# Optimization experiments

Hardware: AMD Instinct MI355X
Metric: run time of the kernel (lower is better)

The kernel has to match this reference:

```python
import jax, jax.numpy as jnp
import numpy as np

BASE_LR = 0.1
LN_EPS = 1e-5
D_IN = 1024
D_OUT = 1024
BATCH = 16384


def setup_inputs() -> dict:
    key = jax.random.key(0)
    ks = jax.random.split(key, 5)
    x = jax.random.normal(ks[0], (BATCH, D_IN), dtype=jnp.float32)
    plasticity = jax.random.uniform(ks[1], (BATCH,), dtype=jnp.float32)
    alpha = jax.random.uniform(ks[2], (1,), dtype=jnp.float32)
    # Parameters / buffers (orthogonal / kaiming init approximated with scaled normals)
    W_slow = jax.random.normal(ks[3], (D_OUT, D_IN), dtype=jnp.float32) * (1.4 / np.sqrt(D_IN))
    bound = 1.0 / np.sqrt(D_IN)  # kaiming_uniform with a=sqrt(5) on [d_out, d_in]
    W_fast = jax.random.uniform(ks[4], (D_OUT, D_IN), dtype=jnp.float32, minval=-bound, maxval=bound)
    gamma = jnp.ones((D_OUT,), dtype=jnp.float32)
    beta = jnp.zeros((D_OUT,), dtype=jnp.float32)
    return {"x": x, "plasticity": plasticity, "alpha": alpha,
            "W_slow": W_slow, "W_fast": W_fast, "gamma": gamma, "beta": beta}


def reference(x, plasticity, alpha, W_slow, W_fast, gamma, beta):
    # Dual linear reads: [B, d_in] @ [d_in, d_out]
    slow = x @ W_slow.T           # [B, d_out]
    fast = x @ W_fast.T           # [B, d_out]

    # Hebbian fast-weight update (training branch, no-grad in original)
    batch = x.shape[0]
    hebb = (fast.T @ x) / batch                         # [d_out, d_in]
    forget = jnp.mean(fast ** 2, axis=0)[:, None] * W_fast  # [d_out, d_in]
    eff_lr = jnp.mean(plasticity) * BASE_LR             # scalar, kept on-device
    W_fast_new = W_fast + jnp.tanh(hebb - forget) * eff_lr

    # Combine + LayerNorm over last dim
    combined = slow + fast * alpha                      # alpha broadcast scalar
    mu = jnp.mean(combined, axis=-1, keepdims=True)
    var = jnp.mean((combined - mu) ** 2, axis=-1, keepdims=True)
    out = (combined - mu) * jax.lax.rsqrt(var + LN_EPS) * gamma + beta
    return (out, slow, W_fast_new)
```

## Files before the change

kernel.cpp:

```cpp
#include <hip/hip_runtime.h>
#include <cstdint>
#include <cstddef>

#define B_SZ 16384
#define DIN  1024
#define DOUT 1024
#define SPLITK 8

typedef short bf16x8 __attribute__((ext_vector_type(8)));
typedef float f32x4  __attribute__((ext_vector_type(4)));

static __device__ __forceinline__ short f2bf(float f) {
    union { float f; unsigned u; } v; v.f = f;
    unsigned r = v.u + 0x7fffu + ((v.u >> 16) & 1u);
    return (short)(r >> 16);
}
static __device__ __forceinline__ float bf2f(short s) {
    union { unsigned u; float f; } v; v.u = ((unsigned)(unsigned short)s) << 16;
    return v.f;
}
static __device__ __forceinline__ void gload_lds16(const short* g, short* l) {
    __builtin_amdgcn_global_load_lds(
        (const __attribute__((address_space(1))) void*)g,
        (__attribute__((address_space(3))) void*)l, 16, 0, 0);
}

__global__ __launch_bounds__(256) void convert_f32_bf16(const float* __restrict__ in,
                                                        short* __restrict__ out, int n4) {
    int i = blockIdx.x * 256 + threadIdx.x;
    if (i < n4) {
        float4 v = ((const float4*)in)[i];
        short4 o;
        o.x = f2bf(v.x); o.y = f2bf(v.y); o.z = f2bf(v.z); o.w = f2bf(v.w);
        ((short4*)out)[i] = o;
    }
}

__global__ __launch_bounds__(256) void x_convert(const float* __restrict__ x,
                                                 short* __restrict__ xb,
                                                 short* __restrict__ xT) {
    __shared__ short t[64 * 72];
    const int b0 = blockIdx.x * 64;
    const int d0 = blockIdx.y * 64;
    const int tid = threadIdx.x;
    const int r = tid >> 2;
    const int c = (tid & 3) * 16;
    short loc[16];
    #pragma unroll
    for (int i = 0; i < 4; ++i) {
        float4 v = *(const float4*)&x[(size_t)(b0 + r) * DIN + d0 + c + i * 4];
        loc[i * 4 + 0] = f2bf(v.x); loc[i * 4 + 1] = f2bf(v.y);
        loc[i * 4 + 2] = f2bf(v.z); loc[i * 4 + 3] = f2bf(v.w);
    }
    *(bf16x8*)&xb[(size_t)(b0 + r) * DIN + d0 + c]     = *(bf16x8*)&loc[0];
    *(bf16x8*)&xb[(size_t)(b0 + r) * DIN + d0 + c + 8] = *(bf16x8*)&loc[8];
    #pragma unroll
    for (int i = 0; i < 16; ++i) t[(c + i) * 72 + r] = loc[i];
    __syncthreads();
    const int d = tid >> 2, bs = (tid & 3) * 16;
    *(bf16x8*)&xT[(size_t)(d0 + d) * B_SZ + b0 + bs]     = *(bf16x8*)&t[d * 72 + bs];
    *(bf16x8*)&xT[(size_t)(d0 + d) * B_SZ + b0 + bs + 8] = *(bf16x8*)&t[d * 72 + bs + 8];
}

__global__ __launch_bounds__(256) void fast_trans(const float* __restrict__ fast,
                                                  short* __restrict__ fastT) {
    __shared__ short t[64 * 72];
    const int b0 = blockIdx.x * 64;
    const int d0 = blockIdx.y * 64;
    const int tid = threadIdx.x;
    const int r = tid >> 2;
    const int c = (tid & 3) * 16;
    short loc[16];
    #pragma unroll
    for (int i = 0; i < 4; ++i) {
        float4 v = *(const float4*)&fast[(size_t)(b0 + r) * DOUT + d0 + c + i * 4];
        loc[i * 4 + 0] = f2bf(v.x); loc[i * 4 + 1] = f2bf(v.y);
        loc[i * 4 + 2] = f2bf(v.z); loc[i * 4 + 3] = f2bf(v.w);
    }
    #pragma unroll
    for (int i = 0; i < 16; ++i) t[(c + i) * 72 + r] = loc[i];
    __syncthreads();
    const int d = tid >> 2, bs = (tid & 3) * 16;
    *(bf16x8*)&fastT[(size_t)(d0 + d) * B_SZ + b0 + bs]     = *(bf16x8*)&t[d * 72 + bs];
    *(bf16x8*)&fastT[(size_t)(d0 + d) * B_SZ + b0 + bs + 8] = *(bf16x8*)&t[d * 72 + bs + 8];
}

__global__ __launch_bounds__(256) void init_kernel(const float* __restrict__ plast,
                                                   float* __restrict__ eff_lr) {
    int tid = threadIdx.x;
    float s = 0.f;
    for (int i = tid; i < B_SZ; i += 256) s += plast[i];
    __shared__ float red[256];
    red[tid] = s; __syncthreads();
    for (int off = 128; off > 0; off >>= 1) {
        if (tid < off) red[tid] += red[tid + off];
        __syncthreads();
    }
    if (tid == 0) eff_lr[0] = (red[0] / (float)B_SZ) * 0.1f;
}

__global__ __launch_bounds__(256) void dual_gemm(
    const short* __restrict__ Xb,
    const short* __restrict__ Wc,
    float* __restrict__ slow_out,
    float* __restrict__ fast_out)
{
    __shared__ short lA[128 * 32];
    __shared__ short lB[128 * 32];
    const int tid = threadIdx.x;
    const int lane = tid & 63;
    const int wave = tid >> 6;
    const int wm = wave & 1, wn = wave >> 1;
    const int quad = lane >> 4, l16 = lane & 15;
    const int m0 = blockIdx.x * 128;
    const int n0 = blockIdx.y * 128;
    const int lrow = lane >> 2;
    const int lcol = (lane & 3) * 8;

    f32x4 acc[4][4] = {};

    const short* gA0 = &Xb[(size_t)(m0 + wave * 32 + lrow) * DIN + lcol];
    const short* gA1 = gA0 + (size_t)16 * DIN;
    const short* gB0 = &Wc[(size_t)(n0 + wave * 32 + lrow) * DIN + lcol];
    const short* gB1 = gB0 + (size_t)16 * DIN;
    short* sA0 = &lA[(wave * 32) * 32];
    short* sA1 = &lA[(wave * 32 + 16) * 32];
    short* sB0 = &lB[(wave * 32) * 32];
    short* sB1 = &lB[(wave * 32 + 16) * 32];

    for (int k0 = 0; k0 < DIN; k0 += 32) {
        gload_lds16(gA0 + k0, sA0);
        gload_lds16(gA1 + k0, sA1);
        gload_lds16(gB0 + k0, sB0);
        gload_lds16(gB1 + k0, sB1);
        __syncthreads();
        bf16x8 af[4], bfr[4];
        #pragma unroll
        for (int t = 0; t < 4; ++t) {
            af[t]  = *(const bf16x8*)&lA[(wm * 64 + t * 16 + l16) * 32 + quad * 8];
            bfr[t] = *(const bf16x8*)&lB[(wn * 64 + t * 16 + l16) * 32 + quad * 8];
        }
        #pragma unroll
        for (int tm = 0; tm < 4; ++tm)
            #pragma unroll
            for (int tn = 0; tn < 4; ++tn)
                acc[tm][tn] = __builtin_amdgcn_mfma_f32_16x16x32_bf16(af[tm], bfr[tn], acc[tm][tn], 0, 0, 0);
        __syncthreads();
    }
    float* dst = (n0 < 1024) ? slow_out : fast_out;
    const int cb = (n0 < 1024) ? n0 : n0 - 1024;
    #pragma unroll
    for (int tm = 0; tm < 4; ++tm) {
        int r0 = m0 + wm * 64 + tm * 16 + quad * 4;
        #pragma unroll
        for (int tn = 0; tn < 4; ++tn) {
            int cc = cb + wn * 64 + tn * 16 + l16;
            #pragma unroll
            for (int r = 0; r < 4; ++r)
                dst[(size_t)(r0 + r) * 1024 + cc] = acc[tm][tn][r];
        }
    }
}

__global__ __launch_bounds__(256) void hebb_gemm(
    const short* __restrict__ fastT,
    const short* __restrict__ xT,
    short* __restrict__ hebb_part)
{
    __shared__ short lA[128 * 32];
    __shared__ short lB[128 * 32];
    const int tid = threadIdx.x;
    const int lane = tid & 63;
    const int wave = tid >> 6;
    const int wm = wave & 1, wn = wave >> 1;
    const int quad = lane >> 4, l16 = lane & 15;
    const int m0 = blockIdx.x * 128;
    const int n0 = blockIdx.y * 128;
    const int kb = blockIdx.z * (B_SZ / SPLITK);
    const int lrow = lane >> 2;
    const int lcol = (lane & 3) * 8;

    f32x4 acc[4][4] = {};

    const short* gA0 = &fastT[(size_t)(m0 + wave * 32 + lrow) * B_SZ + kb + lcol];
    const short* gA1 = gA0 + (size_t)16 * B_SZ;
    const short* gB0 = &xT[(size_t)(n0 + wave * 32 + lrow) * B_SZ + kb + lcol];
    const short* gB1 = gB0 + (size_t)16 * B_SZ;
    short* sA0 = &lA[(wave * 32) * 32];
    short* sA1 = &lA[(wave * 32 + 16) * 32];
    short* sB0 = &lB[(wave * 32) * 32];
    short* sB1 = &lB[(wave * 32 + 16) * 32];

    for (int k0 = 0; k0 < B_SZ / SPLITK; k0 += 32) {
        gload_lds16(gA0 + k0, sA0);
        gload_lds16(gA1 + k0, sA1);
        gload_lds16(gB0 + k0, sB0);
        gload_lds16(gB1 + k0, sB1);
        __syncthreads();
        bf16x8 af[4], bfr[4];
        #pragma unroll
        for (int t = 0; t < 4; ++t) {
            af[t]  = *(const bf16x8*)&lA[(wm * 64 + t * 16 + l16) * 32 + quad * 8];
            bfr[t] = *(const bf16x8*)&lB[(wn * 64 + t * 16 + l16) * 32 + quad * 8];
        }
        #pragma unroll
        for (int tm = 0; tm < 4; ++tm)
            #pragma unroll
            for (int tn = 0; tn < 4; ++tn)
                acc[tm][tn] = __builtin_amdgcn_mfma_f32_16x16x32_bf16(af[tm], bfr[tn], acc[tm][tn], 0, 0, 0);
        __syncthreads();
    }
    short* dst = hebb_part + (size_t)blockIdx.z * DOUT * DIN;
    #pragma unroll
    for (int tm = 0; tm < 4; ++tm) {
        int r0 = m0 + wm * 64 + tm * 16 + quad * 4;
        #pragma unroll
        for (int tn = 0; tn < 4; ++tn) {
            int cc = n0 + wn * 64 + tn * 16 + l16;
            #pragma unroll
            for (int r = 0; r < 4; ++r)
                dst[(size_t)(r0 + r) * DIN + cc] = f2bf(acc[tm][tn][r]);
        }
    }
}

__global__ __launch_bounds__(256) void colsumsq_kernel(const short* __restrict__ fastT,
                                                       float* __restrict__ sums) {
    const int m = blockIdx.x;
    const int tid = threadIdx.x;
    const short* row = &fastT[(size_t)m * B_SZ];
    float s = 0.f;
    for (int i = tid * 8; i < B_SZ; i += 256 * 8) {
        bf16x8 v = *(const bf16x8*)&row[i];
        #pragma unroll
        for (int j = 0; j < 8; ++j) { float f = bf2f(v[j]); s += f * f; }
    }
    __shared__ float red[256];
    red[tid] = s; __syncthreads();
    for (int off = 128; off > 0; off >>= 1) {
        if (tid < off) red[tid] += red[tid + off];
        __syncthreads();
    }
    if (tid == 0) sums[m] = red[0];
}

__global__ __launch_bounds__(256) void wfast_update(
    const float* __restrict__ Wf, const short* __restrict__ hebb_part,
    const float* __restrict__ colsumsq, const float* __restrict__ eff_lr,
    float* __restrict__ Wf_new)
{
    const int i0 = (blockIdx.x * 256 + threadIdx.x) * 8;
    const int m = i0 >> 10;
    const float lr = eff_lr[0];
    const float fgm = colsumsq[m] * (1.0f / (float)B_SZ);
    float h[8] = {0.f, 0.f, 0.f, 0.f, 0.f, 0.f, 0.f, 0.f};
    #pragma unroll
    for (int z = 0; z < SPLITK; ++z) {
        bf16x8 v = *(const bf16x8*)&hebb_part[(size_t)z * DOUT * DIN + i0];
        #pragma unroll
        for (int j = 0; j < 8; ++j) h[j] += bf2f(v[j]);
    }
    float4 w0 = *(const float4*)&Wf[i0];
    float4 w1 = *(const float4*)&Wf[i0 + 4];
    float w[8] = {w0.x, w0.y, w0.z, w0.w, w1.x, w1.y, w1.z, w1.w};
    float o[8];
    #pragma unroll
    for (int j = 0; j < 8; ++j)
        o[j] = w[j] + tanhf(h[j] * (1.0f / (float)B_SZ) - fgm * w[j]) * lr;
    *(float4*)&Wf_new[i0]     = make_float4(o[0], o[1], o[2], o[3]);
    *(float4*)&Wf_new[i0 + 4] = make_float4(o[4], o[5], o[6], o[7]);
}

__global__ __launch_bounds__(256) void ln_kernel(
    const float* __restrict__ slow, float* __restrict__ io,
    const float* __restrict__ gamma, const float* __restrict__ beta,
    const float* __restrict__ alpha)
{
    const int row = blockIdx.x;
    const int tid = threadIdx.x;
    const float a = alpha[0];
    const size_t base = (size_t)row * DOUT;
    float c[4];
    float s = 0.f, ss = 0.f;
    #pragma unroll
    for (int i = 0; i < 4; ++i) {
        int col = tid + i * 256;
        float v = slow[base + col] + a * io[base + col];
        c[i] = v; s += v; ss += v * v;
    }
    #pragma unroll
    for (int off = 32; off > 0; off >>= 1) {
        s  += __shfl_down(s, off);
        ss += __shfl_down(ss, off);
    }
    __shared__ float rs[4], rss[4];
    int wave = tid >> 6;
    if ((tid & 63) == 0) { rs[wave] = s; rss[wave] = ss; }
    __syncthreads();
    float S  = rs[0] + rs[1] + rs[2] + rs[3];
    float SS = rss[0] + rss[1] + rss[2] + rss[3];
    float mu = S * (1.0f / DOUT);
    float var = SS * (1.0f / DOUT) - mu * mu;
    float inv = rsqrtf(var + 1e-5f);
    #pragma unroll
    for (int i = 0; i < 4; ++i) {
        int col = tid + i * 256;
        io[base + col] = (c[i] - mu) * inv * gamma[col] + beta[col];
    }
}

extern "C" void kernel_launch(void* const* d_in, const int* in_sizes, int n_in,
                              void* d_out, int out_size, void* d_ws, size_t ws_size,
                              hipStream_t stream)
{
    const float* x     = (const float*)d_in[0];
    const float* plast = (const float*)d_in[1];
    const float* alpha = (const float*)d_in[2];
    const float* Wslow = (const float*)d_in[3];
    const float* Wfast = (const float*)d_in[4];
    const float* gamma = (const float*)d_in[5];
    const float* beta  = (const float*)d_in[6];

    float* out   = (float*)d_out;
    float* slow  = out + (size_t)B_SZ * DOUT;
    float* wfnew = slow + (size_t)B_SZ * DOUT;

    char* ws = (char*)d_ws;
    short* xb    = (short*)ws;
    short* fastT = xb;
    short* xT    = (short*)(ws + (size_t)B_SZ * DIN * 2);
    short* wcat  = xT + (size_t)DIN * B_SZ;
    short* hebb  = wcat + (size_t)2048 * DIN;
    float* csq   = (float*)(hebb + (size_t)SPLITK * DOUT * DIN);
    float* efflr = csq + DOUT;

    x_convert<<<dim3(B_SZ / 64, DIN / 64), 256, 0, stream>>>(x, xb, xT);
    convert_f32_bf16<<<(DOUT * DIN / 4 + 255) / 256, 256, 0, stream>>>(Wslow, wcat, DOUT * DIN / 4);
    convert_f32_bf16<<<(DOUT * DIN / 4 + 255) / 256, 256, 0, stream>>>(Wfast, wcat + (size_t)DOUT * DIN, DOUT * DIN / 4);
    init_kernel<<<1, 256, 0, stream>>>(plast, efflr);
    dual_gemm<<<dim3(B_SZ / 128, 2048 / 128), 256, 0, stream>>>(xb, wcat, slow, out);
    fast_trans<<<dim3(B_SZ / 64, DOUT / 64), 256, 0, stream>>>(out, fastT);
    colsumsq_kernel<<<DOUT, 256, 0, stream>>>(fastT, csq);
    hebb_gemm<<<dim3(DOUT / 128, DIN / 128, SPLITK), 256, 0, stream>>>(fastT, xT, hebb);
    wfast_update<<<(DOUT * DIN) / (256 * 8), 256, 0, stream>>>(Wfast, hebb, csq, efflr, wfnew);
    ln_kernel<<<B_SZ, 256, 0, stream>>>(slow, out, gamma, beta, alpha);
}
```

Baseline: 435.8 us.

## Fuse fast transpose, column sum-of-squares and alpha-combine into the dual GEMM epilogue

Adds a dual GEMM in which each block computes matching slow and fast tiles together. Its epilogue writes slow, the combined slow+alpha*fast, a transposed bf16 copy of fast, and atomically accumulated column sums of squares. This removes the fast_trans and colsumsq kernels and the reread of fast by LayerNorm, which now normalizes the combined buffer in place. The path runs only when the workspace is large enough for a separate fastT buffer, and it adds atomics plus strided short4 transposed stores.

```diff
diff --git a/kernel.cpp b/kernel.cpp
--- a/kernel.cpp
+++ b/kernel.cpp
@@ -86,8 +86,10 @@
 }
 
 __global__ __launch_bounds__(256) void init_kernel(const float* __restrict__ plast,
-                                                   float* __restrict__ eff_lr) {
+                                                   float* __restrict__ eff_lr,
+                                                   float* __restrict__ csq) {
     int tid = threadIdx.x;
+    for (int i = tid; i < DOUT; i += 256) csq[i] = 0.f;
     float s = 0.f;
     for (int i = tid; i < B_SZ; i += 256) s += plast[i];
     __shared__ float red[256];
@@ -159,6 +161,95 @@
             for (int r = 0; r < 4; ++r)
                 dst[(size_t)(r0 + r) * 1024 + cc] = acc[tm][tn][r];
         }
+    }
+}
+
+__global__ __launch_bounds__(256) void dual_gemm_fused(
+    const short* __restrict__ Xb,
+    const short* __restrict__ Wc,
+    float* __restrict__ slow_out,
+    float* __restrict__ comb_out,
+    short* __restrict__ fastT,
+    float* __restrict__ csq,
+    const float* __restrict__ alpha)
+{
+    __shared__ short lA[128 * 32];
+    __shared__ short lB[128 * 32];
+    const int tid = threadIdx.x;
+    const int lane = tid & 63;
+    const int wave = tid >> 6;
+    const int wm = wave & 1, wn = wave >> 1;
+    const int quad = lane >> 4, l16 = lane & 15;
+    const int m0 = blockIdx.x * 128;
+    const int n0 = blockIdx.y * 64;
+    const int lrow = lane >> 2;
+    const int lcol = (lane & 3) * 8;
+
+    f32x4 accS[4][2] = {};
+    f32x4 accF[4][2] = {};
+
+    const short* gA0 = &Xb[(size_t)(m0 + wave * 32 + lrow) * DIN + lcol];
+    const short* gA1 = gA0 + (size_t)16 * DIN;
+    const int brow = (wave < 2) ? (n0 + wave * 32 + lrow)
+                                : (1024 + n0 + (wave - 2) * 32 + lrow);
+    const short* gB0 = &Wc[(size_t)brow * DIN + lcol];
+    const short* gB1 = gB0 + (size_t)16 * DIN;
+    short* sA0 = &lA[(wave * 32) * 32];
+    short* sA1 = &lA[(wave * 32 + 16) * 32];
+    short* sB0 = &lB[(wave * 32) * 32];
+    short* sB1 = &lB[(wave * 32 + 16) * 32];
+
+    for (int k0 = 0; k0 < DIN; k0 += 32) {
+        gload_lds16(gA0 + k0, sA0);
+        gload_lds16(gA1 + k0, sA1);
+        gload_lds16(gB0 + k0, sB0);
+        gload_lds16(gB1 + k0, sB1);
+        __syncthreads();
+        bf16x8 af[4], bs[2], bff[2];
+        #pragma unroll
+        for (int t = 0; t < 4; ++t)
+            af[t]  = *(const bf16x8*)&lA[(wm * 64 + t * 16 + l16) * 32 + quad * 8];
+        #pragma unroll
+        for (int t = 0; t < 2; ++t) {
+            bs[t]  = *(const bf16x8*)&lB[(wn * 32 + t * 16 + l16) * 32 + quad * 8];
+            bff[t] = *(const bf16x8*)&lB[(64 + wn * 32 + t * 16 + l16) * 32 + quad * 8];
+        }
+        #pragma unroll
+        for (int tm = 0; tm < 4; ++tm)
+            #pragma unroll
+            for (int tn = 0; tn < 2; ++tn) {
+                accS[tm][tn] = __builtin_amdgcn_mfma_f32_16x16x32_bf16(af[tm], bs[tn],  accS[tm][tn], 0, 0, 0);
+                accF[tm][tn] = __builtin_amdgcn_mfma_f32_16x16x32_bf16(af[tm], bff[tn], accF[tm][tn], 0, 0, 0);
+            }
+        __syncthreads();
+    }
+
+    const float a = alpha[0];
+    float cp0 = 0.f, cp1 = 0.f;
+    #pragma unroll
+    for (int tm = 0; tm < 4; ++tm) {
+        const int r0 = m0 + wm * 64 + tm * 16 + quad * 4;
+        #pragma unroll
+        for (int tn = 0; tn < 2; ++tn) {
+            const int cc = n0 + wn * 32 + tn * 16 + l16;
+            short4 s4;
+            #pragma unroll
+            for (int r = 0; r < 4; ++r) {
+                const float fs = accS[tm][tn][r];
+                const float ff = accF[tm][tn][r];
+                slow_out[(size_t)(r0 + r) * 1024 + cc] = fs;
+                comb_out[(size_t)(r0 + r) * 1024 + cc] = fs + a * ff;
+                if (tn == 0) cp0 += ff * ff; else cp1 += ff * ff;
+                ((short*)&s4)[r] = f2bf(ff);
+            }
+            *(short4*)&fastT[(size_t)cc * B_SZ + r0] = s4;
+        }
+    }
+    cp0 += __shfl_xor(cp0, 16); cp0 += __shfl_xor(cp0, 32);
+    cp1 += __shfl_xor(cp1, 16); cp1 += __shfl_xor(cp1, 32);
+    if (quad == 0) {
+        atomicAdd(&csq[n0 + wn * 32 + l16], cp0);
+        atomicAdd(&csq[n0 + wn * 32 + 16 + l16], cp1);
     }
 }
 
@@ -309,6 +400,42 @@
     }
 }
 
+__global__ __launch_bounds__(256) void ln_fused(
+    float* __restrict__ io,
+    const float* __restrict__ gamma, const float* __restrict__ beta)
+{
+    const int row = blockIdx.x;
+    const int tid = threadIdx.x;
+    const size_t base = (size_t)row * DOUT;
+    float c[4];
+    float s = 0.f, ss = 0.f;
+    #pragma unroll
+    for (int i = 0; i < 4; ++i) {
+        int col = tid + i * 256;
+        float v = io[base + col];
+        c[i] = v; s += v; ss += v * v;
+    }
+    #pragma unroll
+    for (int off = 32; off > 0; off >>= 1) {
+        s  += __shfl_down(s, off);
+        ss += __shfl_down(ss, off);
+    }
+    __shared__ float rs[4], rss[4];
+    int wave = tid >> 6;
+    if ((tid & 63) == 0) { rs[wave] = s; rss[wave] = ss; }
+    __syncthreads();
+    float S  = rs[0] + rs[1] + rs[2] + rs[3];
+    float SS = rss[0] + rss[1] + rss[2] + rss[3];
+    float mu = S * (1.0f / DOUT);
+    float var = SS * (1.0f / DOUT) - mu * mu;
+    float inv = rsqrtf(var + 1e-5f);
+    #pragma unroll
+    for (int i = 0; i < 4; ++i) {
+        int col = tid + i * 256;
+        io[base + col] = (c[i] - mu) * inv * gamma[col] + beta[col];
+    }
+}
+
 extern "C" void kernel_launch(void* const* d_in, const int* in_sizes, int n_in,
                               void* d_out, int out_size, void* d_ws, size_t ws_size,
                               hipStream_t stream)
@@ -326,22 +453,51 @@
     float* wfnew = slow + (size_t)B_SZ * DOUT;
 
     char* ws = (char*)d_ws;
-    short* xb    = (short*)ws;
-    short* fastT = xb;
-    short* xT    = (short*)(ws + (size_t)B_SZ * DIN * 2);
-    short* wcat  = xT + (size_t)DIN * B_SZ;
-    short* hebb  = wcat + (size_t)2048 * DIN;
-    float* csq   = (float*)(hebb + (size_t)SPLITK * DOUT * DIN);
-    float* efflr = csq + DOUT;
-
-    x_convert<<<dim3(B_SZ / 64, DIN / 64), 256, 0, stream>>>(x, xb, xT);
-    convert_f32_bf16<<<(DOUT * DIN / 4 + 255) / 256, 256, 0, stream>>>(Wslow, wcat, DOUT * DIN / 4);
-    convert_f32_bf16<<<(DOUT * DIN / 4 + 255) / 256, 256, 0, stream>>>(Wfast, wcat + (size_t)DOUT * DIN, DOUT * DIN / 4);
-    init_kernel<<<1, 256, 0, stream>>>(plast, efflr);
-    dual_gemm<<<dim3(B_SZ / 128, 2048 / 128), 256, 0, stream>>>(xb, wcat, slow, out);
-    fast_trans<<<dim3(B_SZ / 64, DOUT / 64), 256, 0, stream>>>(out, fastT);
-    colsumsq_kernel<<<DOUT, 256, 0, stream>>>(fastT, csq);
-    hebb_gemm<<<dim3(DOUT / 128, DIN / 128, SPLITK), 256, 0, stream>>>(fastT, xT, hebb);
-    wfast_update<<<(DOUT * DIN) / (256 * 8), 256, 0, stream>>>(Wfast, hebb, csq, efflr, wfnew);
-    ln_kernel<<<B_SZ, 256, 0, stream>>>(slow, out, gamma, beta, alpha);
-}
+    const size_t SZ_XB   = (size_t)B_SZ * DIN * 2;
+    const size_t SZ_XT   = (size_t)DIN * B_SZ * 2;
+    const size_t SZ_WCAT = (size_t)2048 * DIN * 2;
+    const size_t SZ_HEBB = (size_t)SPLITK * DOUT * DIN * 2;
+    const size_t SZ_FT   = (size_t)DOUT * B_SZ * 2;
+
+    const size_t need_fused = SZ_XB + SZ_XT + SZ_WCAT + SZ_HEBB + SZ_FT + 4096 + 256;
+    const bool fused = (ws_size >= need_fused);
+
+    if (fused) {
+        short* xb    = (short*)ws;
+        short* xT    = (short*)(ws + SZ_XB);
+        short* wcat  = (short*)(ws + SZ_XB + SZ_XT);
+        short* hebb  = (short*)(ws + SZ_XB + SZ_XT + SZ_WCAT);
+        short* fastT = (short*)(ws + SZ_XB + SZ_XT + SZ_WCAT + SZ_HEBB);
+        float* csq   = (float*)(ws + SZ_XB + SZ_XT + SZ_WCAT + SZ_HEBB + SZ_FT);
+        float* efflr = csq + DOUT;
+
+        x_convert<<<dim3(B_SZ / 64, DIN / 64), 256, 0, stream>>>(x, xb, xT);
+        convert_f32_bf16<<<(DOUT * DIN / 4 + 255) / 256, 256, 0, stream>>>(Wslow, wcat, DOUT * DIN / 4);
+        convert_f32_bf16<<<(DOUT * DIN / 4 + 255) / 256, 256, 0, stream>>>(Wfast, wcat + (size_t)DOUT * DIN, DOUT * DIN / 4);
+        init_kernel<<<1, 256, 0, stream>>>(plast, efflr, csq);
+        dual_gemm_fused<<<dim3(B_SZ / 128, 1024 / 64), 256, 0, stream>>>(
+            xb, wcat, slow, out, fastT, csq, alpha);
+        hebb_gemm<<<dim3(DOUT / 128, DIN / 128, SPLITK), 256, 0, stream>>>(fastT, xT, hebb);
+        wfast_update<<<(DOUT * DIN) / (256 * 8), 256, 0, stream>>>(Wfast, hebb, csq, efflr, wfnew);
+        ln_fused<<<B_SZ, 256, 0, stream>>>(out, gamma, beta);
+    } else {
+        short* xb    = (short*)ws;
+        short* fastT = xb;
+        short* xT    = (short*)(ws + SZ_XB);
+        short* wcat  = (short*)(ws + SZ_XB + SZ_XT);
+        short* hebb  = (short*)(ws + SZ_XB + SZ_XT + SZ_WCAT);
+        float* csq   = (float*)(ws + SZ_XB + SZ_XT + SZ_WCAT + SZ_HEBB);
+        float* efflr = csq + DOUT;
+
+        x_convert<<<dim3(B_SZ / 64, DIN / 64), 256, 0, stream>>>(x, xb, xT);
+        convert_f32_bf16<<<(DOUT * DIN / 4 + 255) / 256, 256, 0, stream>>>(Wslow, wcat, DOUT * DIN / 4);
+        convert_f32_bf16<<<(DOUT * DIN / 4 + 255) / 256, 256, 0, stream>>>(Wfast, wcat + (size_t)DOUT * DIN, DOUT * DIN / 4);
+        init_kernel<<<1, 256, 0, stream>>>(plast, efflr, csq);
+        dual_gemm<<<dim3(B_SZ / 128, 2048 / 128), 256, 0, stream>>>(xb, wcat, slow, out);
+        fast_trans<<<dim3(B_SZ / 64, DOUT / 64), 256, 0, stream>>>(out, fastT);
+        colsumsq_kernel<<<DOUT, 256, 0, stream>>>(fastT, csq);
+        hebb_gemm<<<dim3(DOUT / 128, DIN / 128, SPLITK), 256, 0, stream>>>(fastT, xT, hebb);
+        wfast_update<<<(DOUT * DIN) / (256 * 8), 256, 0, stream>>>(Wfast, hebb, csq, efflr, wfnew);
+        ln_kernel<<<B_SZ, 256, 0, stream>>>(slow, out, gamma, beta, alpha);
+    }
+}
```

Measured after the change: 451.8 us. 3.7% more time.

## Replace both GEMMs with a 256x256 double-buffered 8-wave MFMA core

Applied to the files above, without the earlier changes.

Both the dual forward GEMM and the Hebbian split-K GEMM now share one 256x256-tile, 512-thread core. It uses 64-wide K stages, double-buffered LDS (128KB) filled by async global-to-LDS loads, an XOR swizzle against bank conflicts, and setprio around the MFMA bursts. The dual GEMM gets a remapped block order for L2 locality, and the Hebbian GEMM moves to SPLITK=16 so the larger tiles still fill the GPU. The goal is more data reuse per tile and overlap of loads with MFMA work. In exchange it uses heavy LDS and many registers, allows only one block per CU, and writes twice as many bf16 partial sums for the wfast_update reduction.

```diff
diff --git a/kernel.cpp b/kernel.cpp
--- a/kernel.cpp
+++ b/kernel.cpp
@@ -5,7 +5,7 @@
 #define B_SZ 16384
 #define DIN  1024
 #define DOUT 1024
-#define SPLITK 8
+#define SPLITK 16
 
 typedef short bf16x8 __attribute__((ext_vector_type(8)));
 typedef float f32x4  __attribute__((ext_vector_type(4)));
@@ -86,8 +86,10 @@
 }
 
 __global__ __launch_bounds__(256) void init_kernel(const float* __restrict__ plast,
-                                                   float* __restrict__ eff_lr) {
+                                                   float* __restrict__ eff_lr,
+                                                   float* __restrict__ csq) {
     int tid = threadIdx.x;
+    for (int i = tid; i < DOUT; i += 256) csq[i] = 0.f;
     float s = 0.f;
     for (int i = tid; i < B_SZ; i += 256) s += plast[i];
     __shared__ float red[256];
@@ -99,129 +101,158 @@
     if (tid == 0) eff_lr[0] = (red[0] / (float)B_SZ) * 0.1f;
 }
 
-__global__ __launch_bounds__(256) void dual_gemm(
-    const short* __restrict__ Xb,
-    const short* __restrict__ Wc,
-    float* __restrict__ slow_out,
-    float* __restrict__ fast_out)
-{
-    __shared__ short lA[128 * 32];
-    __shared__ short lB[128 * 32];
-    const int tid = threadIdx.x;
+#define PRIO1 __builtin_amdgcn_s_setprio(1)
+#define PRIO0 __builtin_amdgcn_s_setprio(0)
+#define BARX  asm volatile("s_barrier" ::: "memory")
+#define LGKM0 asm volatile("s_waitcnt lgkmcnt(0)" ::: "memory")
+#define VMC4  asm volatile("s_waitcnt vmcnt(4)" ::: "memory")
+#define VMC0  asm volatile("s_waitcnt vmcnt(0)" ::: "memory")
+
+#define STG(RO, SRC, LD, KT, H) do { \
+    const short* _s = (SRC) + (size_t)((H) * 128 + srow) * (LD) + (KT) * 64 + scol; \
+    gload_lds16(_s, &L[(RO) + ((H) * 128 + wrow8) * 64]); \
+    gload_lds16(_s + (size_t)64 * (LD), &L[(RO) + ((H) * 128 + 64 + wrow8) * 64]); \
+} while (0)
+
+#define RDA(RO, MH) do { \
+    const int _rb = (RO) + (wm * 128 + (MH) * 64 + l16) * 64 + qx; \
+    _Pragma("unroll") for (int mf = 0; mf < 4; ++mf) { \
+        a_[mf][0] = *(const bf16x8*)&L[_rb + mf * 1024]; \
+        a_[mf][1] = *(const bf16x8*)&L[_rb + mf * 1024 + 32]; \
+    } \
+} while (0)
+
+#define RDB(RO, NH) do { \
+    const int _rb = (RO) + (wn * 64 + (NH) * 32 + l16) * 64 + qx; \
+    _Pragma("unroll") for (int nf = 0; nf < 2; ++nf) { \
+        b_[NH][nf][0] = *(const bf16x8*)&L[_rb + nf * 1024]; \
+        b_[NH][nf][1] = *(const bf16x8*)&L[_rb + nf * 1024 + 32]; \
+    } \
+} while (0)
+
+#define MM(MH, NH) do { \
+    _Pragma("unroll") for (int mf = 0; mf < 4; ++mf) \
+    _Pragma("unroll") for (int nf = 0; nf < 2; ++nf) { \
+        acc[(MH)*4+mf][(NH)*2+nf] = __builtin_amdgcn_mfma_f32_16x16x32_bf16(a_[mf][0], b_[NH][nf][0], acc[(MH)*4+mf][(NH)*2+nf], 0, 0, 0); \
+        acc[(MH)*4+mf][(NH)*2+nf] = __builtin_amdgcn_mfma_f32_16x16x32_bf16(a_[mf][1], b_[NH][nf][1], acc[(MH)*4+mf][(NH)*2+nf], 0, 0, 0); \
+    } \
+} while (0)
+
+template<int EPI>
+static __device__ __forceinline__ void gemm256_core(
+    const short* __restrict__ Asrc, int lda,
+    const short* __restrict__ Bsrc, int ldb,
+    float* __restrict__ dstf,
+    short* __restrict__ dsth,
+    int m0, int cb)
+{
+    __shared__ short L[65536];
+    const int A0o = 0, A1o = 16384, B0o = 32768, B1o = 49152;
+    const int tid  = threadIdx.x;
     const int lane = tid & 63;
-    const int wave = tid >> 6;
-    const int wm = wave & 1, wn = wave >> 1;
-    const int quad = lane >> 4, l16 = lane & 15;
-    const int m0 = blockIdx.x * 128;
-    const int n0 = blockIdx.y * 128;
-    const int lrow = lane >> 2;
-    const int lcol = (lane & 3) * 8;
-
-    f32x4 acc[4][4] = {};
-
-    const short* gA0 = &Xb[(size_t)(m0 + wave * 32 + lrow) * DIN + lcol];
-    const short* gA1 = gA0 + (size_t)16 * DIN;
-    const short* gB0 = &Wc[(size_t)(n0 + wave * 32 + lrow) * DIN + lcol];
-    const short* gB1 = gB0 + (size_t)16 * DIN;
-    short* sA0 = &lA[(wave * 32) * 32];
-    short* sA1 = &lA[(wave * 32 + 16) * 32];
-    short* sB0 = &lB[(wave * 32) * 32];
-    short* sB1 = &lB[(wave * 32 + 16) * 32];
-
-    for (int k0 = 0; k0 < DIN; k0 += 32) {
-        gload_lds16(gA0 + k0, sA0);
-        gload_lds16(gA1 + k0, sA1);
-        gload_lds16(gB0 + k0, sB0);
-        gload_lds16(gB1 + k0, sB1);
-        __syncthreads();
-        bf16x8 af[4], bfr[4];
+    const int w    = tid >> 6;
+    const int wm   = w >> 2;
+    const int wn   = w & 3;
+    const int quad = lane >> 4;
+    const int l16  = lane & 15;
+    const int qx   = (quad * 8) ^ ((lane & 4) ? 16 : 0);
+    const int wrow8 = w * 8;
+    const int srow  = tid >> 3;
+    const int scol  = ((lane & 7) * 8) ^ ((lane & 32) >> 1);
+
+    f32x4 acc[8][4] = {};
+    bf16x8 a_[4][2];
+    bf16x8 b_[2][2][2];
+
+    STG(B0o, Bsrc, ldb, 0, 0); STG(B0o, Bsrc, ldb, 0, 1);
+    STG(A0o, Asrc, lda, 0, 0); STG(A0o, Asrc, lda, 0, 1);
+    STG(B1o, Bsrc, ldb, 1, 0); STG(B1o, Bsrc, ldb, 1, 1);
+    VMC4; BARX;
+
+    for (int it = 0; it < 7; ++it) {
+        const int t = 2 * it;
+        RDA(A0o, 0); RDB(B0o, 0); STG(A1o, Asrc, lda, t + 1, 0);
+        BARX; LGKM0; PRIO1; MM(0, 0); PRIO0; BARX;
+        RDB(B0o, 1); STG(A1o, Asrc, lda, t + 1, 1);
+        BARX; LGKM0; PRIO1; MM(0, 1); PRIO0; BARX;
+        RDA(A0o, 1); STG(B0o, Bsrc, ldb, t + 2, 0);
+        BARX; LGKM0; PRIO1; MM(1, 1); PRIO0; BARX;
+        STG(B0o, Bsrc, ldb, t + 2, 1);
+        BARX; PRIO1; MM(1, 0); PRIO0; VMC4; BARX;
+        RDA(A1o, 0); RDB(B1o, 0); STG(A0o, Asrc, lda, t + 2, 0);
+        BARX; LGKM0; PRIO1; MM(0, 0); PRIO0; BARX;
+        RDB(B1o, 1); STG(A0o, Asrc, lda, t + 2, 1);
+        BARX; LGKM0; PRIO1; MM(0, 1); PRIO0; BARX;
+        RDA(A1o, 1); STG(B1o, Bsrc, ldb, t + 3, 0);
+        BARX; LGKM0; PRIO1; MM(1, 1); PRIO0; BARX;
+        STG(B1o, Bsrc, ldb, t + 3, 1);
+        BARX; PRIO1; MM(1, 0); PRIO0; VMC4; BARX;
+    }
+    RDA(A0o, 0); RDB(B0o, 0); STG(A1o, Asrc, lda, 15, 0);
+    BARX; LGKM0; PRIO1; MM(0, 0); PRIO0; BARX;
+    RDB(B0o, 1); STG(A1o, Asrc, lda, 15, 1);
+    BARX; LGKM0; PRIO1; MM(0, 1); PRIO0; BARX;
+    RDA(A0o, 1);
+    BARX; LGKM0; PRIO1; MM(1, 1); PRIO0; BARX;
+    BARX; PRIO1; MM(1, 0); PRIO0; VMC0; BARX;
+    RDA(A1o, 0); RDB(B1o, 0);
+    BARX; LGKM0; PRIO1; MM(0, 0); PRIO0; BARX;
+    RDB(B1o, 1);
+    BARX; LGKM0; PRIO1; MM(0, 1); PRIO0; BARX;
+    RDA(A1o, 1);
+    BARX; LGKM0; PRIO1; MM(1, 1); PRIO0; BARX;
+    PRIO1; MM(1, 0); PRIO0;
+
+    if (EPI == 0) {
         #pragma unroll
-        for (int t = 0; t < 4; ++t) {
-            af[t]  = *(const bf16x8*)&lA[(wm * 64 + t * 16 + l16) * 32 + quad * 8];
-            bfr[t] = *(const bf16x8*)&lB[(wn * 64 + t * 16 + l16) * 32 + quad * 8];
+        for (int mf = 0; mf < 8; ++mf) {
+            const int r0 = m0 + wm * 128 + mf * 16 + quad * 4;
+            #pragma unroll
+            for (int nf = 0; nf < 4; ++nf) {
+                const int cc = cb + wn * 64 + nf * 16 + l16;
+                #pragma unroll
+                for (int r = 0; r < 4; ++r)
+                    dstf[(size_t)(r0 + r) * 1024 + cc] = acc[mf][nf][r];
+            }
         }
+    } else {
         #pragma unroll
-        for (int tm = 0; tm < 4; ++tm)
+        for (int mf = 0; mf < 8; ++mf) {
+            const int r0 = m0 + wm * 128 + mf * 16 + quad * 4;
             #pragma unroll
-            for (int tn = 0; tn < 4; ++tn)
-                acc[tm][tn] = __builtin_amdgcn_mfma_f32_16x16x32_bf16(af[tm], bfr[tn], acc[tm][tn], 0, 0, 0);
-        __syncthreads();
-    }
+            for (int nf = 0; nf < 4; ++nf) {
+                const int cc = cb + wn * 64 + nf * 16 + l16;
+                #pragma unroll
+                for (int r = 0; r < 4; ++r)
+                    dsth[(size_t)(r0 + r) * DIN + cc] = f2bf(acc[mf][nf][r]);
+            }
+        }
+    }
+}
+
+__global__ __launch_bounds__(512) void dual_gemm8(
+    const short* __restrict__ Xb, const short* __restrict__ Wc,
+    float* __restrict__ slow_out, float* __restrict__ fast_out)
+{
+    const int bid = blockIdx.x;
+    const int id  = (bid & 7) * 64 + (bid >> 3);
+    const int bm  = id & 63, bn = id >> 6;
+    const int m0  = bm * 256, n0 = bn * 256;
     float* dst = (n0 < 1024) ? slow_out : fast_out;
-    const int cb = (n0 < 1024) ? n0 : n0 - 1024;
-    #pragma unroll
-    for (int tm = 0; tm < 4; ++tm) {
-        int r0 = m0 + wm * 64 + tm * 16 + quad * 4;
-        #pragma unroll
-        for (int tn = 0; tn < 4; ++tn) {
-            int cc = cb + wn * 64 + tn * 16 + l16;
-            #pragma unroll
-            for (int r = 0; r < 4; ++r)
-                dst[(size_t)(r0 + r) * 1024 + cc] = acc[tm][tn][r];
-        }
-    }
-}
-
-__global__ __launch_bounds__(256) void hebb_gemm(
-    const short* __restrict__ fastT,
-    const short* __restrict__ xT,
+    gemm256_core<0>(&Xb[(size_t)m0 * DIN], DIN, &Wc[(size_t)n0 * DIN], DIN,
+                    dst, nullptr, m0, n0 & 1023);
+}
+
+__global__ __launch_bounds__(512) void hebb_gemm8(
+    const short* __restrict__ fastT, const short* __restrict__ xT,
     short* __restrict__ hebb_part)
 {
-    __shared__ short lA[128 * 32];
-    __shared__ short lB[128 * 32];
-    const int tid = threadIdx.x;
-    const int lane = tid & 63;
-    const int wave = tid >> 6;
-    const int wm = wave & 1, wn = wave >> 1;
-    const int quad = lane >> 4, l16 = lane & 15;
-    const int m0 = blockIdx.x * 128;
-    const int n0 = blockIdx.y * 128;
-    const int kb = blockIdx.z * (B_SZ / SPLITK);
-    const int lrow = lane >> 2;
-    const int lcol = (lane & 3) * 8;
-
-    f32x4 acc[4][4] = {};
-
-    const short* gA0 = &fastT[(size_t)(m0 + wave * 32 + lrow) * B_SZ + kb + lcol];
-    const short* gA1 = gA0 + (size_t)16 * B_SZ;
-    const short* gB0 = &xT[(size_t)(n0 + wave * 32 + lrow) * B_SZ + kb + lcol];
-    const short* gB1 = gB0 + (size_t)16 * B_SZ;
-    short* sA0 = &lA[(wave * 32) * 32];
-    short* sA1 = &lA[(wave * 32 + 16) * 32];
-    short* sB0 = &lB[(wave * 32) * 32];
-    short* sB1 = &lB[(wave * 32 + 16) * 32];
-
-    for (int k0 = 0; k0 < B_SZ / SPLITK; k0 += 32) {
-        gload_lds16(gA0 + k0, sA0);
-        gload_lds16(gA1 + k0, sA1);
-        gload_lds16(gB0 + k0, sB0);
-        gload_lds16(gB1 + k0, sB1);
-        __syncthreads();
-        bf16x8 af[4], bfr[4];
-        #pragma unroll
-        for (int t = 0; t < 4; ++t) {
-            af[t]  = *(const bf16x8*)&lA[(wm * 64 + t * 16 + l16) * 32 + quad * 8];
-            bfr[t] = *(const bf16x8*)&lB[(wn * 64 + t * 16 + l16) * 32 + quad * 8];
-        }
-        #pragma unroll
-        for (int tm = 0; tm < 4; ++tm)
-            #pragma unroll
-            for (int tn = 0; tn < 4; ++tn)
-                acc[tm][tn] = __builtin_amdgcn_mfma_f32_16x16x32_bf16(af[tm], bfr[tn], acc[tm][tn], 0, 0, 0);
-        __syncthreads();
-    }
-    short* dst = hebb_part + (size_t)blockIdx.z * DOUT * DIN;
-    #pragma unroll
-    for (int tm = 0; tm < 4; ++tm) {
-        int r0 = m0 + wm * 64 + tm * 16 + quad * 4;
-        #pragma unroll
-        for (int tn = 0; tn < 4; ++tn) {
-            int cc = n0 + wn * 64 + tn * 16 + l16;
-            #pragma unroll
-            for (int r = 0; r < 4; ++r)
-                dst[(size_t)(r0 + r) * DIN + cc] = f2bf(acc[tm][tn][r]);
-        }
-    }
+    const int m0 = blockIdx.x * 256;
+    const int n0 = blockIdx.y * 256;
+    const size_t kb = (size_t)blockIdx.z * (B_SZ / SPLITK);
+    gemm256_core<1>(&fastT[(size_t)m0 * B_SZ + kb], B_SZ,
+                    &xT[(size_t)n0 * B_SZ + kb], B_SZ,
+                    nullptr, hebb_part + (size_t)blockIdx.z * DOUT * DIN, m0, n0);
 }
 
 __global__ __launch_bounds__(256) void colsumsq_kernel(const short* __restrict__ fastT,
@@ -326,22 +357,26 @@
     float* wfnew = slow + (size_t)B_SZ * DOUT;
 
     char* ws = (char*)d_ws;
+    const size_t SZ_XB   = (size_t)B_SZ * DIN * 2;
+    const size_t SZ_XT   = (size_t)DIN * B_SZ * 2;
+    const size_t SZ_WCAT = (size_t)2048 * DIN * 2;
+    const size_t SZ_HEBB = (size_t)SPLITK * DOUT * DIN * 2;
     short* xb    = (short*)ws;
     short* fastT = xb;
-    short* xT    = (short*)(ws + (size_t)B_SZ * DIN * 2);
-    short* wcat  = xT + (size_t)DIN * B_SZ;
-    short* hebb  = wcat + (size_t)2048 * DIN;
-    float* csq   = (float*)(hebb + (size_t)SPLITK * DOUT * DIN);
+    short* xT    = (short*)(ws + SZ_XB);
+    short* wcat  = (short*)(ws + SZ_XB + SZ_XT);
+    short* hebb  = (short*)(ws + SZ_XB + SZ_XT + SZ_WCAT);
+    float* csq   = (float*)(ws + SZ_XB + SZ_XT + SZ_WCAT + SZ_HEBB);
     float* efflr = csq + DOUT;
 
     x_convert<<<dim3(B_SZ / 64, DIN / 64), 256, 0, stream>>>(x, xb, xT);
     convert_f32_bf16<<<(DOUT * DIN / 4 + 255) / 256, 256, 0, stream>>>(Wslow, wcat, DOUT * DIN / 4);
     convert_f32_bf16<<<(DOUT * DIN / 4 + 255) / 256, 256, 0, stream>>>(Wfast, wcat + (size_t)DOUT * DIN, DOUT * DIN / 4);
-    init_kernel<<<1, 256, 0, stream>>>(plast, efflr);
-    dual_gemm<<<dim3(B_SZ / 128, 2048 / 128), 256, 0, stream>>>(xb, wcat, slow, out);
+    init_kernel<<<1, 256, 0, stream>>>(plast, efflr, csq);
+    dual_gemm8<<<512, 512, 0, stream>>>(xb, wcat, slow, out);
     fast_trans<<<dim3(B_SZ / 64, DOUT / 64), 256, 0, stream>>>(out, fastT);
     colsumsq_kernel<<<DOUT, 256, 0, stream>>>(fastT, csq);
-    hebb_gemm<<<dim3(DOUT / 128, DIN / 128, SPLITK), 256, 0, stream>>>(fastT, xT, hebb);
+    hebb_gemm8<<<dim3(DOUT / 256, DIN / 256, SPLITK), 512, 0, stream>>>(fastT, xT, hebb);
     wfast_update<<<(DOUT * DIN) / (256 * 8), 256, 0, stream>>>(Wfast, hebb, csq, efflr, wfnew);
     ln_kernel<<<B_SZ, 256, 0, stream>>>(slow, out, gamma, beta, alpha);
 }
```

After: 405.1 us. -7.0%, faster.
